# Performance work log

Measured on AMD Instinct MI355X. Metric: run time of the kernel, lower is better.

## Reference

```python
import jax, jax.numpy as jnp
import numpy as np

L = 3          # num_layers
HID = 256      # hidden_size
NF = 16        # num_features_params
TF = NF + 1    # total_features
B = 128
T = 256
EPS = 1e-5     # torch LayerNorm default


def _ln(x, g, b):
    mu = jnp.mean(x, axis=-1, keepdims=True)
    var = jnp.mean((x - mu) ** 2, axis=-1, keepdims=True)
    return (x - mu) * jax.lax.rsqrt(var + EPS) * g + b


def setup_inputs() -> dict:
    key = jax.random.key(0)
    ks = iter(jax.random.split(key, 64))
    w = lambda *s: jax.random.normal(next(ks), s, dtype=jnp.float32) * 0.05
    d = {
        'parameters_input': jax.random.normal(next(ks), (B, NF), dtype=jnp.float32),
        'displacement_input': jax.random.normal(next(ks), (B, T), dtype=jnp.float32),
        # input_embed: Linear(TF,H) + LayerNorm(H)
        'embed_w': w(TF, HID), 'embed_b': w(HID),
        'embed_g': jnp.ones((HID,), jnp.float32), 'embed_beta': jnp.zeros((HID,), jnp.float32),
        # skip_connection: Linear(TF, H//2)
        'skip_w': w(TF, HID // 2), 'skip_b': w(HID // 2),
        # per-layer LSTM cell params, stacked over L
        'gates_w': w(L, 2 * HID, 4 * HID), 'gates_b': w(L, 4 * HID),
        'inln_g': jnp.ones((L, HID), jnp.float32), 'inln_b': jnp.zeros((L, HID), jnp.float32),
        'hln_g': jnp.ones((L, HID), jnp.float32), 'hln_b': jnp.zeros((L, HID), jnp.float32),
        'sln_g': jnp.ones((L, HID), jnp.float32), 'sln_b': jnp.zeros((L, HID), jnp.float32),
        'aw1': w(L, HID, HID), 'ab1': w(L, HID),
        'aw2': w(L, HID, 1), 'ab2': w(L, 1),
        # per-layer residual blocks: Linear(H,2H), Linear(2H,H), LayerNorm(H)
        'rw1': w(L, HID, 2 * HID), 'rb1': w(L, 2 * HID),
        'rw2': w(L, 2 * HID, HID), 'rb2': w(L, HID),
        'rln_g': jnp.ones((L, HID), jnp.float32), 'rln_b': jnp.zeros((L, HID), jnp.float32),
        # output head: Linear(H + H//2, H//2) [bug-fixed in_features], LayerNorm, Linear(H//2,1)
        'ow1': w(HID + HID // 2, HID // 2), 'ob1': w(HID // 2),
        'oln_g': jnp.ones((HID // 2,), jnp.float32), 'oln_b': jnp.zeros((HID // 2,), jnp.float32),
        'ow2': w(HID // 2, 1), 'ob2': w(1),
    }
    return d


def _forward(parameters_input, displacement_input, embed_w, embed_b, embed_g, embed_beta,
             skip_w, skip_b, gates_w, gates_b, inln_g, inln_b, hln_g, hln_b, sln_g, sln_b,
             aw1, ab1, aw2, ab2, rw1, rb1, rw2, rb2, rln_g, rln_b,
             ow1, ob1, oln_g, oln_b, ow2, ob2):
    Bb, Tt = displacement_input.shape
    # [B,T,TF]: displacement as extra feature at index 0, params broadcast over time
    seq = jnp.concatenate([
        displacement_input[..., None],
        jnp.broadcast_to(parameters_input[:, None, :], (Bb, Tt, parameters_input.shape[1])),
    ], axis=-1)
    xs = jnp.swapaxes(seq, 0, 1)  # [T,B,TF]
    h0 = jnp.zeros((L, Bb, HID), seq.dtype)
    c0 = jnp.zeros((L, Bb, HID), seq.dtype)

    def step(carry, xt):
        h_all, c_all = carry
        skip = jax.nn.relu(xt @ skip_w + skip_b)                      # [B,H/2]
        x = jax.nn.relu(_ln(xt @ embed_w + embed_b, embed_g, embed_beta))
        hs, cs = [], []
        for l in range(L):
            residual = x
            h, c = h_all[l], c_all[l]
            xn = _ln(x, inln_g[l], inln_b[l])
            hn = _ln(h, hln_g[l], hln_b[l])
            g4 = jnp.concatenate([xn, hn], axis=-1) @ gates_w[l] + gates_b[l]
            i, f, g, o = jnp.split(g4, 4, axis=-1)
            i = jax.nn.sigmoid(i); f = jax.nn.sigmoid(f)
            g = jnp.tanh(g); o = jax.nn.sigmoid(o)
            imp = jax.nn.sigmoid(jnp.tanh(c @ aw1[l] + ab1[l]) @ aw2[l] + ab2[l])  # [B,1]
            c = _ln((f * c + i * g) * imp, sln_g[l], sln_b[l])
            h = o * jnp.tanh(c)
            hs.append(h); cs.append(c)
            x = h
            rb = jax.nn.relu(x @ rw1[l] + rb1[l]) @ rw2[l] + rb2[l]
            x = _ln(rb + x, rln_g[l], rln_b[l]) + residual
        y = jnp.concatenate([x, skip], axis=-1)                        # [B, H + H/2]
        out = jax.nn.relu(_ln(y @ ow1 + ob1, oln_g, oln_b)) @ ow2 + ob2  # [B,1]
        return (jnp.stack(hs), jnp.stack(cs)), out[:, 0]

    _, outs = jax.lax.scan(step, (h0, c0), xs)   # outs [T,B]
    return jnp.swapaxes(outs, 0, 1)              # [B,T]


def reference(parameters_input, displacement_input, embed_w, embed_b, embed_g, embed_beta,
              skip_w, skip_b, gates_w, gates_b, inln_g, inln_b, hln_g, hln_b, sln_g, sln_b,
              aw1, ab1, aw2, ab2, rw1, rb1, rw2, rb2, rln_g, rln_b,
              ow1, ob1, oln_g, oln_b, ow2, ob2):
    return _forward(parameters_input, displacement_input, embed_w, embed_b, embed_g, embed_beta,
                    skip_w, skip_b, gates_w, gates_b, inln_g, inln_b, hln_g, hln_b, sln_g, sln_b,
                    aw1, ab1, aw2, ab2, rw1, rb1, rw2, rb2, rln_g, rln_b,
                    ow1, ob1, oln_g, oln_b, ow2, ob2)
```

## Files before the change

### kernel.cpp

```cpp
#include <hip/hip_runtime.h>
#include <cstdint>

#define TT 256
#define HH 256
#define LL 3
#define NTH 512
#define SWG 8
#define CLN 32
#define RW 4
#define LN_EPS 1e-5f
#define ACTSTRIDE 16384


__device__ __forceinline__ float fast_sigmoid(float x) {
    return 1.f / (1.f + __expf(-x));
}
__device__ __forceinline__ float fast_tanh(float x) {
    float xc = fminf(fmaxf(x, -15.f), 15.f);
    float e = __expf(2.f * xc);
    return 1.f - 2.f / (e + 1.f);
}
__device__ __forceinline__ float relu(float x) { return fmaxf(x, 0.f); }

__device__ __forceinline__ void cst(float* p, float v) {
    __hip_atomic_store(p, v, __ATOMIC_RELAXED, __HIP_MEMORY_SCOPE_AGENT);
}
__device__ __forceinline__ float cld(const float* p) {
    return __hip_atomic_load(p, __ATOMIC_RELAXED, __HIP_MEMORY_SCOPE_AGENT);
}

__device__ __forceinline__ float4 rowsum4(float s0, float q0, float s1, float q1,
                                          float* scr, int tid) {
#pragma unroll
    for (int o = 32; o > 0; o >>= 1) {
        s0 += __shfl_down(s0, o); q0 += __shfl_down(q0, o);
        s1 += __shfl_down(s1, o); q1 += __shfl_down(q1, o);
    }
    int w = tid >> 6;
    if ((tid & 63) == 0) { scr[w*4] = s0; scr[w*4+1] = q0; scr[w*4+2] = s1; scr[w*4+3] = q1; }
    __syncthreads();
    int base = (tid >> 8) * 16;
    float sA = 0, qA = 0, sB = 0, qB = 0;
#pragma unroll
    for (int i = 0; i < 4; i++) {
        sA += scr[base + i*4];     qA += scr[base + i*4 + 1];
        sB += scr[base + i*4 + 2]; qB += scr[base + i*4 + 3];
    }
    __syncthreads();
    return make_float4(sA, qA, sB, qB);
}

__device__ __forceinline__ float2 red2head(float a, float b, float* scr, int tid) {
#pragma unroll
    for (int o = 32; o > 0; o >>= 1) {
        a += __shfl_down(a, o);
        b += __shfl_down(b, o);
    }
    int w = tid >> 6;
    if ((tid & 63) == 0) { scr[w] = a; scr[8 + w] = b; }
    __syncthreads();
    int r = tid >> 7;
    float2 out = make_float2(scr[2*r] + scr[2*r+1], scr[8+2*r] + scr[8+2*r+1]);
    __syncthreads();
    return out;
}

__device__ __forceinline__ void fma16(float4 w, float4 x,
                                      float4& a0, float4& a1, float4& a2, float4& a3) {
    a0.x = fmaf(w.x, x.x, a0.x); a0.y = fmaf(w.y, x.x, a0.y);
    a0.z = fmaf(w.z, x.x, a0.z); a0.w = fmaf(w.w, x.x, a0.w);
    a1.x = fmaf(w.x, x.y, a1.x); a1.y = fmaf(w.y, x.y, a1.y);
    a1.z = fmaf(w.z, x.y, a1.z); a1.w = fmaf(w.w, x.y, a1.w);
    a2.x = fmaf(w.x, x.z, a2.x); a2.y = fmaf(w.y, x.z, a2.y);
    a2.z = fmaf(w.z, x.z, a2.z); a2.w = fmaf(w.w, x.z, a2.w);
    a3.x = fmaf(w.x, x.w, a3.x); a3.y = fmaf(w.y, x.w, a3.y);
    a3.z = fmaf(w.z, x.w, a3.z); a3.w = fmaf(w.w, x.w, a3.w);
}


struct Args {
    const float *params, *disp;
    const float *embed_b, *embed_g, *embed_beta;
    const float *skip_b;
    const float *gates_b;
    const float *inln_g, *inln_b, *hln_g, *hln_b, *sln_g, *sln_b;
    const float *ab1, *aw2, *ab2;
    const float *rb1, *rb2, *rln_g, *rln_b;
    const float *ob1, *oln_g, *oln_b, *ow2, *ob2;
    const float *gw, *a1w, *r1w, *r2w, *ew, *sw, *o1w;
    float* out;
    float* act;
    int* bar;
};

__global__ __launch_bounds__(NTH) void xlstm_kernel(Args A) {
    const int tid = threadIdx.x;
    const int cid = blockIdx.x & 31;
    const int m   = blockIdx.x >> 5;
    const int n   = tid & 255;
    const int p   = tid >> 8;
    const int rA = p, rB = p + 2;

    float* gatesB = A.act + (size_t)cid * ACTSTRIDE;
    float* a1B  = gatesB + 4096;
    float* r2P  = gatesB + 4224;
    float* o1B  = gatesB + 12416;
    int* myflag = A.bar + cid * 128 + m * 16;

    __shared__ __align__(16) float4 P4[2064];
    __shared__ __align__(16) float4 xnhnT[512];
    __shared__ __align__(16) float4 cT4[256];
    __shared__ __align__(16) float4 hT4[256];
    __shared__ __align__(16) float4 xT4[256];
    __shared__ __align__(16) float4 skT4[128];
    __shared__ __align__(16) float4 r1locT[64];
    __shared__ float xtT[17 * 4];
    __shared__ float scr[64];

    float x2[2] = {0.f, 0.f};
    float h2[LL][2] = {{0.f,0.f},{0.f,0.f},{0.f,0.f}};
    float c2[LL][2] = {{0.f,0.f},{0.f,0.f},{0.f,0.f}};

    int ep = 0;
    auto csig = [&]() {
        ep++;
        __syncthreads();
        if (tid == 0)
            __hip_atomic_store(myflag, ep, __ATOMIC_RELAXED, __HIP_MEMORY_SCOPE_AGENT);
    };
    auto cwait = [&]() {
        if (tid == 0) {
#pragma unroll 1
            for (int mm = 0; mm < SWG; mm++) {
                const int* f = A.bar + cid * 128 + mm * 16;
                while (__hip_atomic_load(f, __ATOMIC_RELAXED, __HIP_MEMORY_SCOPE_AGENT) < ep)
                    __builtin_amdgcn_s_sleep(4);
            }
            asm volatile("" ::: "memory");
        }
        __syncthreads();
    };

    if (tid < 64) {
        int k = tid >> 2, rr = tid & 3;
        xtT[(1 + k) * 4 + rr] = A.params[(RW * cid + rr) * 16 + k];
    }
    if (tid < 4) xtT[tid] = A.disp[(RW * cid + tid) * TT + 0];
    __syncthreads();

    for (int t = 0; t < TT; t++) {
        float e0 = A.embed_b[n], e1 = e0;
#pragma unroll 4
        for (int k = 0; k < 17; k++) {
            float w = A.ew[k * 256 + n];
            e0 = fmaf(w, xtT[k * 4 + rA], e0);
            e1 = fmaf(w, xtT[k * 4 + rB], e1);
        }
        {
            int mm = tid & 127, q = tid >> 7;
            float s = A.skip_b[mm];
#pragma unroll 4
            for (int k = 0; k < 17; k++) s = fmaf(A.sw[k * 128 + mm], xtT[k * 4 + q], s);
            ((float*)&skT4[mm])[q] = relu(s);
        }
        float4 rs = rowsum4(e0, e0 * e0, e1, e1 * e1, scr, tid);
        {
            float mu = rs.x * (1.f/HH), inv = rsqrtf(rs.y * (1.f/HH) - mu*mu + LN_EPS);
            x2[0] = relu((e0 - mu) * inv * A.embed_g[n] + A.embed_beta[n]);
            mu = rs.z * (1.f/HH); inv = rsqrtf(rs.w * (1.f/HH) - mu*mu + LN_EPS);
            x2[1] = relu((e1 - mu) * inv * A.embed_g[n] + A.embed_beta[n]);
        }

#pragma unroll 1
        for (int l = 0; l < LL; l++) {
            rs = rowsum4(x2[0], x2[0]*x2[0], x2[1], x2[1]*x2[1], scr, tid);
            {
                const float* g = A.inln_g + l*HH; const float* b = A.inln_b + l*HH;
                float mu = rs.x*(1.f/HH), inv = rsqrtf(rs.y*(1.f/HH) - mu*mu + LN_EPS);
                ((float*)&xnhnT[n])[rA] = (x2[0] - mu) * inv * g[n] + b[n];
                mu = rs.z*(1.f/HH); inv = rsqrtf(rs.w*(1.f/HH) - mu*mu + LN_EPS);
                ((float*)&xnhnT[n])[rB] = (x2[1] - mu) * inv * g[n] + b[n];
            }
            float hA = h2[l][0], hB = h2[l][1];
            rs = rowsum4(hA, hA*hA, hB, hB*hB, scr, tid);
            {
                const float* g = A.hln_g + l*HH; const float* b = A.hln_b + l*HH;
                float mu = rs.x*(1.f/HH), inv = rsqrtf(rs.y*(1.f/HH) - mu*mu + LN_EPS);
                ((float*)&xnhnT[256 + n])[rA] = (hA - mu) * inv * g[n] + b[n];
                mu = rs.z*(1.f/HH); inv = rsqrtf(rs.w*(1.f/HH) - mu*mu + LN_EPS);
                ((float*)&xnhnT[256 + n])[rB] = (hB - mu) * inv * g[n] + b[n];
            }
            ((float*)&cT4[n])[rA] = c2[l][0];
            ((float*)&cT4[n])[rB] = c2[l][1];
            __syncthreads();

            {
                int j = tid & 31, kg = tid >> 5;
                const float4* Wq = (const float4*)A.gw + (size_t)l*512*256 + (m*32 + j);
                float4 a0={0,0,0,0}, a1v={0,0,0,0}, a2={0,0,0,0}, a3={0,0,0,0};
                int k0 = kg * 32;
#pragma unroll 8
                for (int kk = 0; kk < 32; kk++) {
                    int k = k0 + kk;
                    fma16(Wq[(size_t)k * 256], xnhnT[k], a0, a1v, a2, a3);
                }
                int b = kg*32 + j;
                P4[b] = a0; P4[516 + b] = a1v; P4[2*516 + b] = a2; P4[3*516 + b] = a3;
            }
            __syncthreads();
            if (tid < 128) {
                int j2 = tid >> 2, row = tid & 3;
                float4 s = {0,0,0,0};
#pragma unroll
                for (int kg = 0; kg < 16; kg++) {
                    float4 v = P4[row*516 + kg*32 + j2];
                    s.x += v.x; s.y += v.y; s.z += v.z; s.w += v.w;
                }
                float* d = gatesB + row*1024 + m*128 + j2*4;
                cst(d+0, s.x); cst(d+1, s.y); cst(d+2, s.z); cst(d+3, s.w);
            }
            __syncthreads();
            if (tid < 256) {
                int j = tid & 7, kg = tid >> 3;
                const float4* Wq = (const float4*)A.a1w + (size_t)l*256*64 + (m*8 + j);
                float4 a0={0,0,0,0}, a1v={0,0,0,0}, a2={0,0,0,0}, a3={0,0,0,0};
                int k0 = kg * 8;
#pragma unroll
                for (int kk = 0; kk < 8; kk++) {
                    int k = k0 + kk;
                    fma16(Wq[(size_t)k * 64], cT4[k], a0, a1v, a2, a3);
                }
                int b = kg*8 + j;
                P4[b] = a0; P4[260 + b] = a1v; P4[2*260 + b] = a2; P4[3*260 + b] = a3;
            }
            __syncthreads();
            if (tid < 32) {
                int j2 = tid >> 2, row = tid & 3;
                float4 s = {0,0,0,0};
#pragma unroll
                for (int kg = 0; kg < 32; kg++) {
                    float4 v = P4[row*260 + kg*8 + j2];
                    s.x += v.x; s.y += v.y; s.z += v.z; s.w += v.w;
                }
                const float* ab1p = A.ab1 + l*HH + m*32 + j2*4;
                const float* aw2p = A.aw2 + l*HH + m*32 + j2*4;
                float d = fast_tanh(s.x + ab1p[0]) * aw2p[0]
                        + fast_tanh(s.y + ab1p[1]) * aw2p[1]
                        + fast_tanh(s.z + ab1p[2]) * aw2p[2]
                        + fast_tanh(s.w + ab1p[3]) * aw2p[3];
                scr[tid] = d;
            }
            __syncthreads();
            if (tid < 4) {
                float s = 0.f;
#pragma unroll
                for (int j2 = 0; j2 < 8; j2++) s += scr[j2*4 + tid];
                cst(a1B + m*4 + tid, s);
            }

            float4 w2[8], w3[8];
            csig();
            {
                int j = tid & 15, kg = tid >> 4, k0 = kg * 8;
                const float4* Wq = (const float4*)A.r1w + (size_t)l*256*128 + (m*16 + j);
#pragma unroll
                for (int kk = 0; kk < 8; kk++) w2[kk] = Wq[(size_t)(k0 + kk) * 128];
                int j3 = tid & 63, kg3 = tid >> 6, k03 = kg3 * 8;
                const float4* Wq3 = (const float4*)A.r2w + (size_t)l*512*64
                                    + (size_t)(m*64) * 64 + j3;
#pragma unroll
                for (int kk = 0; kk < 8; kk++) w3[kk] = Wq3[(size_t)(k03 + kk) * 64];
            }
            cwait();

            float imp0, imp1;
            {
                float sA = A.ab2[l], sB = A.ab2[l];
#pragma unroll
                for (int mm = 0; mm < SWG; mm++) {
                    sA += cld(a1B + mm*4 + rA);
                    sB += cld(a1B + mm*4 + rB);
                }
                imp0 = fast_sigmoid(sA); imp1 = fast_sigmoid(sB);
            }
            const float* gb = A.gates_b + l*1024;
            float craw0, craw1, og0, og1;
            {
                const float* go = gatesB + rA*1024;
                float ii = fast_sigmoid(cld(go + n) + gb[n]);
                float ff = fast_sigmoid(cld(go + 256 + n) + gb[256+n]);
                float gg = fast_tanh(cld(go + 512 + n) + gb[512+n]);
                og0 = fast_sigmoid(cld(go + 768 + n) + gb[768+n]);
                craw0 = (ff * c2[l][0] + ii * gg) * imp0;
            }
            {
                const float* go = gatesB + rB*1024;
                float ii = fast_sigmoid(cld(go + n) + gb[n]);
                float ff = fast_sigmoid(cld(go + 256 + n) + gb[256+n]);
                float gg = fast_tanh(cld(go + 512 + n) + gb[512+n]);
                og1 = fast_sigmoid(cld(go + 768 + n) + gb[768+n]);
                craw1 = (ff * c2[l][1] + ii * gg) * imp1;
            }
            rs = rowsum4(craw0, craw0*craw0, craw1, craw1*craw1, scr, tid);
            {
                const float* g = A.sln_g + l*HH; const float* b = A.sln_b + l*HH;
                float mu = rs.x*(1.f/HH), inv = rsqrtf(rs.y*(1.f/HH) - mu*mu + LN_EPS);
                float cn = (craw0 - mu) * inv * g[n] + b[n];
                c2[l][0] = cn; float hh = og0 * fast_tanh(cn);
                h2[l][0] = hh; ((float*)&hT4[n])[rA] = hh;
                mu = rs.z*(1.f/HH); inv = rsqrtf(rs.w*(1.f/HH) - mu*mu + LN_EPS);
                cn = (craw1 - mu) * inv * g[n] + b[n];
                c2[l][1] = cn; hh = og1 * fast_tanh(cn);
                h2[l][1] = hh; ((float*)&hT4[n])[rB] = hh;
            }
            __syncthreads();

            {
                int j = tid & 15, kg = tid >> 4;
                float4 a0={0,0,0,0}, a1v={0,0,0,0}, a2={0,0,0,0}, a3={0,0,0,0};
                int k0 = kg * 8;
#pragma unroll
                for (int kk = 0; kk < 8; kk++)
                    fma16(w2[kk], hT4[k0 + kk], a0, a1v, a2, a3);
                int b = kg*16 + j;
                P4[b] = a0; P4[516 + b] = a1v; P4[2*516 + b] = a2; P4[3*516 + b] = a3;
            }
            __syncthreads();
            if (tid < 64) {
                int j2 = tid >> 2, row = tid & 3;
                float4 s = {0,0,0,0};
#pragma unroll
                for (int kg = 0; kg < 32; kg++) {
                    float4 v = P4[row*516 + kg*16 + j2];
                    s.x += v.x; s.y += v.y; s.z += v.z; s.w += v.w;
                }
                const float* rb1p = A.rb1 + l*512 + m*64 + j2*4;
                ((float*)&r1locT[j2*4 + 0])[row] = relu(s.x + rb1p[0]);
                ((float*)&r1locT[j2*4 + 1])[row] = relu(s.y + rb1p[1]);
                ((float*)&r1locT[j2*4 + 2])[row] = relu(s.z + rb1p[2]);
                ((float*)&r1locT[j2*4 + 3])[row] = relu(s.w + rb1p[3]);
            }
            __syncthreads();

            {
                int j = tid & 63, kg = tid >> 6;
                float4 a0={0,0,0,0}, a1v={0,0,0,0}, a2={0,0,0,0}, a3={0,0,0,0};
                int k0 = kg * 8;
#pragma unroll
                for (int kk = 0; kk < 8; kk++) {
                    int lk = k0 + kk;
                    fma16(w3[kk], r1locT[lk], a0, a1v, a2, a3);
                }
                int b = kg*64 + j;
                P4[b] = a0; P4[516 + b] = a1v; P4[2*516 + b] = a2; P4[3*516 + b] = a3;
            }
            __syncthreads();
            {
                int j2 = tid >> 2, row = tid & 3;
                if (tid < 256) {
                    float4 s = {0,0,0,0};
#pragma unroll
                    for (int kg = 0; kg < 8; kg++) {
                        float4 v = P4[row*516 + kg*64 + j2];
                        s.x += v.x; s.y += v.y; s.z += v.z; s.w += v.w;
                    }
                    float* d = r2P + m*1024 + row*256 + j2*4;
                    cst(d+0, s.x); cst(d+1, s.y); cst(d+2, s.z); cst(d+3, s.w);
                }
            }
            csig(); cwait();

            const float* rb2p = A.rb2 + l*HH;
            float s0 = rb2p[n] + h2[l][0];
            float s1 = rb2p[n] + h2[l][1];
#pragma unroll
            for (int mm = 0; mm < SWG; mm++) {
                s0 += cld(r2P + mm*1024 + rA*256 + n);
                s1 += cld(r2P + mm*1024 + rB*256 + n);
            }
            rs = rowsum4(s0, s0*s0, s1, s1*s1, scr, tid);
            {
                const float* g = A.rln_g + l*HH; const float* b = A.rln_b + l*HH;
                float mu = rs.x*(1.f/HH), inv = rsqrtf(rs.y*(1.f/HH) - mu*mu + LN_EPS);
                x2[0] = (s0 - mu) * inv * g[n] + b[n] + x2[0];
                mu = rs.z*(1.f/HH); inv = rsqrtf(rs.w*(1.f/HH) - mu*mu + LN_EPS);
                x2[1] = (s1 - mu) * inv * g[n] + b[n] + x2[1];
            }
        }

        ((float*)&xT4[n])[rA] = x2[0];
        ((float*)&xT4[n])[rB] = x2[1];
        if (tid < 4 && t < TT - 1)
            xtT[tid] = A.disp[(RW * cid + tid) * TT + t + 1];
        __syncthreads();
        {
            int j = tid & 3, kg = tid >> 2;
            const float4* Wq = (const float4*)A.o1w + (m*4 + j);
            float4 a0={0,0,0,0}, a1v={0,0,0,0}, a2={0,0,0,0}, a3={0,0,0,0};
            int k0 = kg * 3;
#pragma unroll
            for (int kk = 0; kk < 3; kk++) {
                int k = k0 + kk;
                float4 x = (k < 256) ? xT4[k] : skT4[k - 256];
                fma16(Wq[(size_t)k * 32], x, a0, a1v, a2, a3);
            }
            int b = kg*4 + j;
            P4[b] = a0; P4[516 + b] = a1v; P4[2*516 + b] = a2; P4[3*516 + b] = a3;
        }
        __syncthreads();
        float* o1S = o1B + (t & 1) * 512;
        if (tid < 16) {
            int j2 = tid >> 2, row = tid & 3;
            float4 s = {0,0,0,0};
#pragma unroll
            for (int kg = 0; kg < 128; kg++) {
                float4 v = P4[row*516 + kg*4 + j2];
                s.x += v.x; s.y += v.y; s.z += v.z; s.w += v.w;
            }
            float* d = o1S + row*128 + m*16 + j2*4;
            cst(d+0, s.x); cst(d+1, s.y); cst(d+2, s.z); cst(d+3, s.w);
        }
        csig();
        if (m == 0) {
            cwait();
            int mm = tid & 127, row = tid >> 7;
            float v = cld(o1S + row*128 + mm) + A.ob1[mm];
            float2 f2 = red2head(v, v * v, scr, tid);
            float mu = f2.x * (1.f/128.f);
            float inv = rsqrtf(f2.y * (1.f/128.f) - mu*mu + LN_EPS);
            float contrib = relu((v - mu) * inv * A.oln_g[mm] + A.oln_b[mm]) * A.ow2[mm];
            f2 = red2head(contrib, 0.f, scr, tid);
            if (mm == 0) A.out[(RW*cid + row) * TT + t] = f2.x + A.ob2[0];
        }
        __syncthreads();
    }
}


extern "C" void kernel_launch(void* const* d_in, const int* in_sizes, int n_in,
                              void* d_out, int out_size, void* d_ws, size_t ws_size,
                              hipStream_t stream) {
    hipMemsetAsync(d_ws, 0, CLN * 128 * sizeof(int), stream);

    Args A;
    A.params     = (const float*)d_in[0];
    A.disp       = (const float*)d_in[1];
    A.ew         = (const float*)d_in[2];
    A.embed_b    = (const float*)d_in[3];
    A.embed_g    = (const float*)d_in[4];
    A.embed_beta = (const float*)d_in[5];
    A.sw         = (const float*)d_in[6];
    A.skip_b     = (const float*)d_in[7];
    A.gw         = (const float*)d_in[8];
    A.gates_b    = (const float*)d_in[9];
    A.inln_g     = (const float*)d_in[10];
    A.inln_b     = (const float*)d_in[11];
    A.hln_g      = (const float*)d_in[12];
    A.hln_b      = (const float*)d_in[13];
    A.sln_g      = (const float*)d_in[14];
    A.sln_b      = (const float*)d_in[15];
    A.a1w        = (const float*)d_in[16];
    A.ab1        = (const float*)d_in[17];
    A.aw2        = (const float*)d_in[18];
    A.ab2        = (const float*)d_in[19];
    A.r1w        = (const float*)d_in[20];
    A.rb1        = (const float*)d_in[21];
    A.r2w        = (const float*)d_in[22];
    A.rb2        = (const float*)d_in[23];
    A.rln_g      = (const float*)d_in[24];
    A.rln_b      = (const float*)d_in[25];
    A.o1w        = (const float*)d_in[26];
    A.ob1        = (const float*)d_in[27];
    A.oln_g      = (const float*)d_in[28];
    A.oln_b      = (const float*)d_in[29];
    A.ow2        = (const float*)d_in[30];
    A.ob2        = (const float*)d_in[31];
    A.out        = (float*)d_out;
    A.bar        = (int*)d_ws;
    A.act        = (float*)d_ws + CLN * 128;

    xlstm_kernel<<<CLN * SWG, NTH, 0, stream>>>(A);
}
```

Before: 24.30 ms.

## Compute output head redundantly per workgroup and replace per-WG flags with shared counter

```diff
diff --git a/kernel.cpp b/kernel.cpp
--- a/kernel.cpp
+++ b/kernel.cpp
@@ -48,21 +48,6 @@
     }
     __syncthreads();
     return make_float4(sA, qA, sB, qB);
-}
-
-__device__ __forceinline__ float2 red2head(float a, float b, float* scr, int tid) {
-#pragma unroll
-    for (int o = 32; o > 0; o >>= 1) {
-        a += __shfl_down(a, o);
-        b += __shfl_down(b, o);
-    }
-    int w = tid >> 6;
-    if ((tid & 63) == 0) { scr[w] = a; scr[8 + w] = b; }
-    __syncthreads();
-    int r = tid >> 7;
-    float2 out = make_float2(scr[2*r] + scr[2*r+1], scr[8+2*r] + scr[8+2*r+1]);
-    __syncthreads();
-    return out;
 }
 
 __device__ __forceinline__ void fma16(float4 w, float4 x,
@@ -104,8 +89,7 @@
     float* gatesB = A.act + (size_t)cid * ACTSTRIDE;
     float* a1B  = gatesB + 4096;
     float* r2P  = gatesB + 4224;
-    float* o1B  = gatesB + 12416;
-    int* myflag = A.bar + cid * 128 + m * 16;
+    int* cnt = A.bar + cid * 128;
 
     __shared__ __align__(16) float4 P4[2064];
     __shared__ __align__(16) float4 xnhnT[512];
@@ -126,16 +110,12 @@
         ep++;
         __syncthreads();
         if (tid == 0)
-            __hip_atomic_store(myflag, ep, __ATOMIC_RELAXED, __HIP_MEMORY_SCOPE_AGENT);
+            __hip_atomic_fetch_add(cnt, 1, __ATOMIC_RELAXED, __HIP_MEMORY_SCOPE_AGENT);
     };
     auto cwait = [&]() {
         if (tid == 0) {
-#pragma unroll 1
-            for (int mm = 0; mm < SWG; mm++) {
-                const int* f = A.bar + cid * 128 + mm * 16;
-                while (__hip_atomic_load(f, __ATOMIC_RELAXED, __HIP_MEMORY_SCOPE_AGENT) < ep)
-                    __builtin_amdgcn_s_sleep(4);
-            }
+            while (__hip_atomic_load(cnt, __ATOMIC_RELAXED, __HIP_MEMORY_SCOPE_AGENT) < SWG * ep)
+                __builtin_amdgcn_s_sleep(4);
             asm volatile("" ::: "memory");
         }
         __syncthreads();
@@ -394,43 +374,52 @@
             xtT[tid] = A.disp[(RW * cid + tid) * TT + t + 1];
         __syncthreads();
         {
-            int j = tid & 3, kg = tid >> 2;
-            const float4* Wq = (const float4*)A.o1w + (m*4 + j);
-            float4 a0={0,0,0,0}, a1v={0,0,0,0}, a2={0,0,0,0}, a3={0,0,0,0};
-            int k0 = kg * 3;
-#pragma unroll
-            for (int kk = 0; kk < 3; kk++) {
+            int j = tid & 31, z = tid >> 5;
+            int row = z & 3, kg = z >> 2;
+            const float4* W4 = (const float4*)A.o1w;
+            float4 a4 = {0,0,0,0};
+            int k0 = kg * 96;
+#pragma unroll 8
+            for (int kk = 0; kk < 96; kk++) {
                 int k = k0 + kk;
-                float4 x = (k < 256) ? xT4[k] : skT4[k - 256];
-                fma16(Wq[(size_t)k * 32], x, a0, a1v, a2, a3);
-            }
-            int b = kg*4 + j;
-            P4[b] = a0; P4[516 + b] = a1v; P4[2*516 + b] = a2; P4[3*516 + b] = a3;
+                float xv = (k < 256) ? ((const float*)&xT4[k])[row]
+                                     : ((const float*)&skT4[k - 256])[row];
+                float4 w = W4[(size_t)k * 32 + j];
+                a4.x = fmaf(w.x, xv, a4.x); a4.y = fmaf(w.y, xv, a4.y);
+                a4.z = fmaf(w.z, xv, a4.z); a4.w = fmaf(w.w, xv, a4.w);
+            }
+            P4[z * 33 + j] = a4;
         }
         __syncthreads();
-        float* o1S = o1B + (t & 1) * 512;
-        if (tid < 16) {
-            int j2 = tid >> 2, row = tid & 3;
-            float4 s = {0,0,0,0};
-#pragma unroll
-            for (int kg = 0; kg < 128; kg++) {
-                float4 v = P4[row*516 + kg*4 + j2];
-                s.x += v.x; s.y += v.y; s.z += v.z; s.w += v.w;
-            }
-            float* d = o1S + row*128 + m*16 + j2*4;
-            cst(d+0, s.x); cst(d+1, s.y); cst(d+2, s.z); cst(d+3, s.w);
-        }
-        csig();
-        if (m == 0) {
-            cwait();
-            int mm = tid & 127, row = tid >> 7;
-            float v = cld(o1S + row*128 + mm) + A.ob1[mm];
-            float2 f2 = red2head(v, v * v, scr, tid);
-            float mu = f2.x * (1.f/128.f);
-            float inv = rsqrtf(f2.y * (1.f/128.f) - mu*mu + LN_EPS);
-            float contrib = relu((v - mu) * inv * A.oln_g[mm] + A.oln_b[mm]) * A.ow2[mm];
-            f2 = red2head(contrib, 0.f, scr, tid);
-            if (mm == 0) A.out[(RW*cid + row) * TT + t] = f2.x + A.ob2[0];
+        if (tid < 128) {
+            int j = tid & 31, row = tid >> 5;
+            float4 v = {0,0,0,0};
+#pragma unroll
+            for (int kg = 0; kg < 4; kg++) {
+                float4 pv = P4[(kg * 4 + row) * 33 + j];
+                v.x += pv.x; v.y += pv.y; v.z += pv.z; v.w += pv.w;
+            }
+            float4 b1 = ((const float4*)A.ob1)[j];
+            v.x += b1.x; v.y += b1.y; v.z += b1.z; v.w += b1.w;
+            float s = v.x + v.y + v.z + v.w;
+            float q = v.x*v.x + v.y*v.y + v.z*v.z + v.w*v.w;
+#pragma unroll
+            for (int o = 16; o > 0; o >>= 1) { s += __shfl_down(s, o); q += __shfl_down(q, o); }
+            s = __shfl(s, tid & 32);
+            q = __shfl(q, tid & 32);
+            float mu = s * (1.f/128.f);
+            float inv = rsqrtf(q * (1.f/128.f) - mu*mu + LN_EPS);
+            float4 g4 = ((const float4*)A.oln_g)[j];
+            float4 be4 = ((const float4*)A.oln_b)[j];
+            float4 w24 = ((const float4*)A.ow2)[j];
+            float part = relu((v.x - mu) * inv * g4.x + be4.x) * w24.x
+                       + relu((v.y - mu) * inv * g4.y + be4.y) * w24.y
+                       + relu((v.z - mu) * inv * g4.z + be4.z) * w24.z
+                       + relu((v.w - mu) * inv * g4.w + be4.w) * w24.w;
+#pragma unroll
+            for (int o = 16; o > 0; o >>= 1) part += __shfl_down(part, o);
+            if (m == 0 && (tid & 31) == 0)
+                A.out[(RW*cid + row) * TT + t] = part + A.ob2[0];
         }
         __syncthreads();
     }
```

Measured after the change: 23.27 ms. -4.2%, faster.
